# Performance work log

Hardware: AMD Instinct MI355X
Metric: run time of the kernel (lower is better)

## Reference

```python
import jax, jax.numpy as jnp
import numpy as np

IN_DIM = 128; OUT_DIM = 128; H = 8; DK = OUT_DIM // H
N_A = 100000; N_B = 100000; E0 = 400000; E1 = 400000
NUM_TYPES = 2; NUM_REL = 2
EPS = 1e-9; LN_EPS = 1e-5


def setup_inputs() -> dict:
    key = jax.random.key(0)
    ks = jax.random.split(key, 16)
    s = 0.02
    xav = float(np.sqrt(6.0 / (DK + DK)))  # xavier_uniform bound for (dk, dk)
    inp = {}
    inp['x_a'] = jax.random.normal(ks[0], (N_A, IN_DIM), jnp.float32)
    inp['x_b'] = jax.random.normal(ks[1], (N_B, IN_DIM), jnp.float32)
    inp['ew0'] = jax.random.uniform(ks[2], (E0,), jnp.float32)
    inp['ew1'] = jax.random.uniform(ks[3], (E1,), jnp.float32)
    inp['src0'] = jax.random.randint(ks[4], (E0,), 0, N_A)
    inp['dst0'] = jax.random.randint(ks[5], (E0,), 0, N_B)
    inp['src1'] = jax.random.randint(ks[6], (E1,), 0, N_B)
    inp['dst1'] = jax.random.randint(ks[7], (E1,), 0, N_A)
    # per-node-type stacked linear params: [type, in, out]
    inp['Wk'] = jax.random.normal(ks[8], (NUM_TYPES, IN_DIM, OUT_DIM), jnp.float32) * s
    inp['bk'] = jnp.zeros((NUM_TYPES, OUT_DIM), jnp.float32)
    inp['Wq'] = jax.random.normal(ks[9], (NUM_TYPES, IN_DIM, OUT_DIM), jnp.float32) * s
    inp['bq'] = jnp.zeros((NUM_TYPES, OUT_DIM), jnp.float32)
    inp['Wv'] = jax.random.normal(ks[10], (NUM_TYPES, IN_DIM, OUT_DIM), jnp.float32) * s
    inp['bv'] = jnp.zeros((NUM_TYPES, OUT_DIM), jnp.float32)
    inp['Wa'] = jax.random.normal(ks[11], (NUM_TYPES, OUT_DIM, OUT_DIM), jnp.float32) * s
    inp['ba'] = jnp.zeros((NUM_TYPES, OUT_DIM), jnp.float32)
    inp['ln_g'] = jnp.ones((NUM_TYPES, OUT_DIM), jnp.float32)
    inp['ln_b'] = jnp.zeros((NUM_TYPES, OUT_DIM), jnp.float32)
    inp['rel_pri'] = jnp.ones((NUM_REL, H), jnp.float32)
    inp['rel_att'] = jax.random.uniform(ks[12], (NUM_REL, H, DK, DK), jnp.float32, -xav, xav)
    inp['rel_msg'] = jax.random.uniform(ks[13], (NUM_REL, H, DK, DK), jnp.float32, -xav, xav)
    inp['skip'] = jnp.ones((NUM_TYPES,), jnp.float32)
    return inp


def _edge_softmax(logits, dst, n_dst):
    # segment softmax over incoming edges of each dst node; logits: (E, H)
    m = jax.ops.segment_max(logits, dst, num_segments=n_dst)
    e = jnp.exp(logits - m[dst])
    s = jax.ops.segment_sum(e, dst, num_segments=n_dst)
    return e / s[dst]


def _relation(x_s, x_d, src, dst, ew, Wk_s, bk_s, Wq_d, bq_d, Wv_s, bv_s,
              ratt, rmsg, rpri, n_dst):
    # per-relation HGT attention -> aggregated dst messages (n_dst, H, DK)
    k = (x_s @ Wk_s + bk_s).reshape(-1, H, DK)
    k = jnp.einsum('nhd,hde->nhe', k, ratt)
    v = (x_s @ Wv_s + bv_s).reshape(-1, H, DK)
    v = jnp.einsum('nhd,hde->nhe', v, rmsg)
    q = (x_d @ Wq_d + bq_d).reshape(-1, H, DK)
    t = jnp.einsum('ehd,ehd->eh', q[dst], k[src])  # edge dot score (E, H)
    # dst-normalized edge weight -> additive log bias
    ew = jnp.clip(ew, 0.0)
    den = jax.ops.segment_sum(ew, dst, num_segments=n_dst)
    ewn = ew / jnp.maximum(den[dst], EPS)
    t = t + jnp.log(ewn + EPS)[:, None]
    t = t * rpri / jnp.sqrt(jnp.float32(DK))
    a = _edge_softmax(t, dst, n_dst)  # (E, H)
    msg = v[src] * a[:, :, None]      # (E, H, DK)
    return jax.ops.segment_sum(msg, dst, num_segments=n_dst)


def _forward(x_a, x_b, ew0, ew1, Wk, bk, Wq, bq, Wv, bv, Wa, ba, ln_g, ln_b,
             rel_pri, rel_att, rel_msg, skip, src0, dst0, src1, dst1):
    # relation 0: a -> b (src type 0, dst type 1); relation 1: b -> a
    t_b = _relation(x_a, x_b, src0, dst0, ew0, Wk[0], bk[0], Wq[1], bq[1],
                    Wv[0], bv[0], rel_att[0], rel_msg[0], rel_pri[0], x_b.shape[0])
    t_a = _relation(x_b, x_a, src1, dst1, ew1, Wk[1], bk[1], Wq[0], bq[0],
                    Wv[1], bv[1], rel_att[1], rel_msg[1], rel_pri[1], x_a.shape[0])
    def combine(t, base, nid):
        alpha = jax.nn.sigmoid(skip[nid])
        trans = t.reshape(-1, OUT_DIM) @ Wa[nid] + ba[nid]  # dropout: eval mode
        out = trans * alpha + base * (1.0 - alpha)
        mu = jnp.mean(out, axis=-1, keepdims=True)
        var = jnp.var(out, axis=-1, keepdims=True)
        return (out - mu) / jnp.sqrt(var + LN_EPS) * ln_g[nid] + ln_b[nid]
    return combine(t_a, x_a, 0), combine(t_b, x_b, 1)


def reference(x_a, x_b, ew0, ew1, src0, dst0, src1, dst1, Wk, bk, Wq, bq, Wv, bv,
              Wa, ba, ln_g, ln_b, rel_pri, rel_att, rel_msg, skip):
    return _forward(x_a, x_b, ew0, ew1, Wk, bk, Wq, bq, Wv, bv, Wa, ba, ln_g, ln_b,
                    rel_pri, rel_att, rel_msg, skip, src0, dst0, src1, dst1)
```

## Files before the change

kernel.cpp:

```cpp
#include <hip/hip_runtime.h>
#include <cstdint>
#include <cstddef>

#define EPSF 1e-9f

typedef __bf16 bf16x8 __attribute__((ext_vector_type(8)));
typedef float fvec4 __attribute__((ext_vector_type(4)));

__device__ __forceinline__ float blo(unsigned int u) { return __uint_as_float(u << 16); }
__device__ __forceinline__ float bhi(unsigned int u) { return __uint_as_float(u & 0xffff0000u); }
__device__ __forceinline__ unsigned short f2bf(float f) {
  unsigned int u = __float_as_uint(f);
  u += 0x7fffu + ((u >> 16) & 1u);
  return (unsigned short)(u >> 16);
}
__device__ __forceinline__ unsigned int pack2bf(float a, float b) {
  return (unsigned int)f2bf(a) | ((unsigned int)f2bf(b) << 16);
}

__global__ __launch_bounds__(256) void fzero(float* __restrict__ p, long n) {
  long i = (long)blockIdx.x * blockDim.x + threadIdx.x;
  long stride = (long)gridDim.x * blockDim.x;
  long n4 = n >> 2;
  float4* p4 = (float4*)p;
  for (long j = i; j < n4; j += stride) p4[j] = make_float4(0.f, 0.f, 0.f, 0.f);
  for (long j = (n4 << 2) + i; j < n; j += stride) p[j] = 0.f;
}

__global__ __launch_bounds__(256) void fuse_w(
    const float* __restrict__ Wk, const float* __restrict__ bk,
    const float* __restrict__ Wv, const float* __restrict__ bv,
    const float* __restrict__ rel_att, const float* __restrict__ rel_msg,
    __bf16* __restrict__ WkvT, float* __restrict__ bkvf)
{
  int i = blockIdx.x;
  int t = blockIdx.y;
  int c = threadIdx.x;
  int m = c >> 7, cc = c & 127;
  int h = cc >> 4, e = cc & 15;
  const float* R = (m ? rel_msg : rel_att) + t * 2048 + h * 256;
  const float* srcW = (m ? Wv : Wk) + t * 16384;
  const float* srcB = (m ? bv : bk) + t * 128;
  const float* row = (i < 128) ? (srcW + i * 128) : srcB;
  float acc = 0.f;
#pragma unroll
  for (int d = 0; d < 16; ++d) acc = fmaf(row[h * 16 + d], R[d * 16 + e], acc);
  if (i < 128) WkvT[(size_t)t * 32768 + (size_t)c * 128 + i] = (__bf16)acc;
  else         bkvf[t * 256 + c] = acc;
}

__global__ __launch_bounds__(128) void cvt_wT(
    const float* __restrict__ Wq, const float* __restrict__ Wa,
    __bf16* __restrict__ WqT, __bf16* __restrict__ WaT)
{
  int k = blockIdx.x, t = blockIdx.y, c = threadIdx.x;
  const float* src = (blockIdx.z ? Wa : Wq) + t * 16384 + k * 128 + c;
  __bf16* dst = (blockIdx.z ? WaT : WqT) + t * 16384 + c * 128 + k;
  dst[0] = (__bf16)src[0];
}

__global__ __launch_bounds__(256) void gemm_mfma(
    const float* __restrict__ A, int M,
    const __bf16* __restrict__ WT, const float* __restrict__ bias,
    __bf16* __restrict__ C, int ldc)
{
  int tid = threadIdx.x, l = tid & 63, wid = tid >> 6;
  int l15 = l & 15, l4 = l >> 4;
  int rowb = blockIdx.x * 64 + (wid & 1) * 32;
  int colb = blockIdx.y * 128 + (wid >> 1) * 64;

  fvec4 z = {0.f, 0.f, 0.f, 0.f};
  fvec4 acc[2][4];
#pragma unroll
  for (int m = 0; m < 2; ++m)
#pragma unroll
    for (int n = 0; n < 4; ++n) acc[m][n] = z;

#pragma unroll
  for (int ks = 0; ks < 4; ++ks) {
    int kb = ks * 32 + l4 * 8;
    bf16x8 af[2], bfr[4];
#pragma unroll
    for (int m = 0; m < 2; ++m) {
      int r = rowb + m * 16 + l15;
      r = r < M ? r : M - 1;
      const float4* ap = (const float4*)(A + (size_t)r * 128 + kb);
      float4 a0 = ap[0], a1 = ap[1];
      bf16x8 v;
      v[0] = (__bf16)a0.x; v[1] = (__bf16)a0.y; v[2] = (__bf16)a0.z; v[3] = (__bf16)a0.w;
      v[4] = (__bf16)a1.x; v[5] = (__bf16)a1.y; v[6] = (__bf16)a1.z; v[7] = (__bf16)a1.w;
      af[m] = v;
    }
#pragma unroll
    for (int n = 0; n < 4; ++n)
      bfr[n] = *(const bf16x8*)(WT + (size_t)(colb + n * 16 + l15) * 128 + kb);
#pragma unroll
    for (int m = 0; m < 2; ++m)
#pragma unroll
      for (int n = 0; n < 4; ++n)
        acc[m][n] = __builtin_amdgcn_mfma_f32_16x16x32_bf16(af[m], bfr[n], acc[m][n], 0, 0, 0);
  }

#pragma unroll
  for (int m = 0; m < 2; ++m)
#pragma unroll
    for (int n = 0; n < 4; ++n) {
      int col = colb + n * 16 + l15;
      float bcol = bias[col];
#pragma unroll
      for (int reg = 0; reg < 4; ++reg) {
        int r = rowb + m * 16 + l4 * 4 + reg;
        if (r < M) C[(size_t)r * ldc + col] = (__bf16)(acc[m][n][reg] + bcol);
      }
    }
}

__global__ __launch_bounds__(256) void csr_count2(
    const int* __restrict__ dst0, int E0, const int* __restrict__ dst1, int E1,
    int* __restrict__ deg, int NB)
{
  int e = blockIdx.x * 256 + threadIdx.x;
  if (e < E0) atomicAdd(&deg[dst0[e]], 1);
  else if (e < E0 + E1) atomicAdd(&deg[NB + dst1[e - E0]], 1);
}

__global__ __launch_bounds__(256) void csr_partial(
    const int* __restrict__ deg, int N, int* __restrict__ partial)
{
  int base = blockIdx.x * 1024 + threadIdx.x * 4;
  int s = 0;
#pragma unroll
  for (int i = 0; i < 4; ++i) if (base + i < N) s += deg[base + i];
#pragma unroll
  for (int m = 1; m < 64; m <<= 1) s += __shfl_xor(s, m, 64);
  __shared__ int wsum[4];
  if ((threadIdx.x & 63) == 0) wsum[threadIdx.x >> 6] = s;
  __syncthreads();
  if (threadIdx.x == 0) partial[blockIdx.x] = wsum[0] + wsum[1] + wsum[2] + wsum[3];
}

__global__ void csr_scan_partials(const int* __restrict__ partial,
                                  int* __restrict__ pscan, int NP)
{
  if (blockIdx.x == 0 && threadIdx.x == 0) {
    int s = 0;
    for (int i = 0; i < NP; ++i) { pscan[i] = s; s += partial[i]; }
  }
}

__global__ __launch_bounds__(256) void csr_scan_chunk(
    const int* __restrict__ deg, const int* __restrict__ pscan,
    int* __restrict__ row_start, int* __restrict__ cursor, int N)
{
  __shared__ int ls[256];
  int base = blockIdx.x * 1024 + threadIdx.x * 4;
  int v0 = 0, v1 = 0, v2 = 0, v3 = 0;
  if (base + 0 < N) v0 = deg[base + 0];
  if (base + 1 < N) v1 = deg[base + 1];
  if (base + 2 < N) v2 = deg[base + 2];
  if (base + 3 < N) v3 = deg[base + 3];
  int s = v0 + v1 + v2 + v3;
  ls[threadIdx.x] = s;
  __syncthreads();
  for (int off = 1; off < 256; off <<= 1) {
    int t = (threadIdx.x >= off) ? ls[threadIdx.x - off] : 0;
    __syncthreads();
    ls[threadIdx.x] += t;
    __syncthreads();
  }
  int excl = pscan[blockIdx.x] + ls[threadIdx.x] - s;
  int p0 = excl, p1 = excl + v0, p2 = excl + v0 + v1, p3 = excl + v0 + v1 + v2;
  if (base + 0 < N) { row_start[base + 0] = p0; cursor[base + 0] = p0; }
  if (base + 1 < N) { row_start[base + 1] = p1; cursor[base + 1] = p1; }
  if (base + 2 < N) { row_start[base + 2] = p2; cursor[base + 2] = p2; }
  if (base + 3 < N) { row_start[base + 3] = p3; cursor[base + 3] = p3; }
}

__global__ __launch_bounds__(256) void csr_scatter2(
    const int* __restrict__ dst0, const int* __restrict__ src0, const float* __restrict__ ew0, int E0,
    const int* __restrict__ dst1, const int* __restrict__ src1, const float* __restrict__ ew1, int E1,
    int* __restrict__ cursor, int* __restrict__ sidx, float* __restrict__ ewc, int NB)
{
  int e = blockIdx.x * 256 + threadIdx.x;
  if (e < E0) {
    int p = atomicAdd(&cursor[dst0[e]], 1);
    sidx[p] = src0[e];
    ewc[p] = fmaxf(ew0[e], 0.f);
  } else if (e < E0 + E1) {
    int e1 = e - E0;
    int p = atomicAdd(&cursor[NB + dst1[e1]], 1);
    sidx[p] = src1[e1];
    ewc[p] = fmaxf(ew1[e1], 0.f);
  }
}

__device__ __forceinline__ void proc_edge(
    float qlo, float qhi, unsigned int ku, unsigned int vu, float w,
    float inv_den, float pr, float& s, float2& acc)
{
  float t = qlo * blo(ku) + qhi * bhi(ku);
  t += __shfl_xor(t, 1, 64);
  t += __shfl_xor(t, 2, 64);
  t += __shfl_xor(t, 4, 64);
  float x = __expf((t + __logf(w * inv_den + EPSF)) * pr);
  s += x;
  acc.x = fmaf(x, blo(vu), acc.x);
  acc.y = fmaf(x, bhi(vu), acc.y);
}

__global__ __launch_bounds__(256) void hgt_dst(
    const __bf16* __restrict__ kvsb, const __bf16* __restrict__ qb,
    const int* __restrict__ row_start, const int* __restrict__ deg,
    const int* __restrict__ sidx, const float* __restrict__ ewc,
    const float* __restrict__ pri8,
    __bf16* __restrict__ agg, int N)
{
  const unsigned short* kvs = (const unsigned short*)kvsb;
  int n = (blockIdx.x * 256 + threadIdx.x) >> 6;
  int lane = threadIdx.x & 63;
  if (n >= N) return;
  int c0 = lane * 2;
  unsigned int* out = (unsigned int*)(agg + (size_t)n * 128 + c0);
  int d = deg[n];
  if (d == 0) { out[0] = 0u; return; }
  int base = row_start[n];

  float ds = 0.f;
  for (int j = lane; j < d; j += 64) ds += ewc[base + j];
#pragma unroll
  for (int m = 1; m < 64; m <<= 1) ds += __shfl_xor(ds, m, 64);
  float inv_den = 1.f / fmaxf(ds, EPSF);

  int h = lane >> 3;
  float pr = pri8[h] * 0.25f;
  unsigned int qu = *(const unsigned int*)((const unsigned short*)qb + (size_t)n * 128 + c0);
  float qlo = blo(qu), qhi = bhi(qu);

  float s = 0.f;
  float2 acc = make_float2(0.f, 0.f);
  int j = 0;
  for (; j + 4 <= d; j += 4) {
    int b = base + j;
    int si0 = sidx[b], si1 = sidx[b + 1], si2 = sidx[b + 2], si3 = sidx[b + 3];
    float w0 = ewc[b], w1 = ewc[b + 1], w2 = ewc[b + 2], w3 = ewc[b + 3];
    const unsigned short* p0 = kvs + (size_t)si0 * 256 + c0;
    const unsigned short* p1 = kvs + (size_t)si1 * 256 + c0;
    const unsigned short* p2 = kvs + (size_t)si2 * 256 + c0;
    const unsigned short* p3 = kvs + (size_t)si3 * 256 + c0;
    unsigned int k0 = *(const unsigned int*)p0, v0 = *(const unsigned int*)(p0 + 128);
    unsigned int k1 = *(const unsigned int*)p1, v1 = *(const unsigned int*)(p1 + 128);
    unsigned int k2 = *(const unsigned int*)p2, v2 = *(const unsigned int*)(p2 + 128);
    unsigned int k3 = *(const unsigned int*)p3, v3 = *(const unsigned int*)(p3 + 128);
    proc_edge(qlo, qhi, k0, v0, w0, inv_den, pr, s, acc);
    proc_edge(qlo, qhi, k1, v1, w1, inv_den, pr, s, acc);
    proc_edge(qlo, qhi, k2, v2, w2, inv_den, pr, s, acc);
    proc_edge(qlo, qhi, k3, v3, w3, inv_den, pr, s, acc);
  }
  for (; j < d; ++j) {
    int b = base + j;
    const unsigned short* p = kvs + (size_t)sidx[b] * 256 + c0;
    proc_edge(qlo, qhi, *(const unsigned int*)p, *(const unsigned int*)(p + 128),
              ewc[b], inv_den, pr, s, acc);
  }
  float is = 1.f / s;
  out[0] = pack2bf(acc.x * is, acc.y * is);
}

__global__ __launch_bounds__(256) void wa_ln(
    const __bf16* __restrict__ Ag, const __bf16* __restrict__ WT,
    const float* __restrict__ bias, const float* __restrict__ xbase,
    const float* __restrict__ g, const float* __restrict__ bb,
    const float* __restrict__ skip, float* __restrict__ out, int M)
{
  int tid = threadIdx.x, l = tid & 63, wid = tid >> 6;
  int l15 = l & 15, l4 = l >> 4;
  int rowb = blockIdx.x * 64 + wid * 16;

  fvec4 z = {0.f, 0.f, 0.f, 0.f};
  fvec4 acc[8];
#pragma unroll
  for (int n = 0; n < 8; ++n) acc[n] = z;

#pragma unroll
  for (int ks = 0; ks < 4; ++ks) {
    int kb = ks * 32 + l4 * 8;
    int r = rowb + l15;
    r = r < M ? r : M - 1;
    bf16x8 af = *(const bf16x8*)(Ag + (size_t)r * 128 + kb);
#pragma unroll
    for (int n = 0; n < 8; ++n) {
      bf16x8 bfr = *(const bf16x8*)(WT + (size_t)(n * 16 + l15) * 128 + kb);
      acc[n] = __builtin_amdgcn_mfma_f32_16x16x32_bf16(af, bfr, acc[n], 0, 0, 0);
    }
  }

  float alpha = 1.f / (1.f + __expf(-skip[0]));
  float onema = 1.f - alpha;
  float o[8][4];
  float psum[4] = {0.f, 0.f, 0.f, 0.f};
  float psq[4] = {0.f, 0.f, 0.f, 0.f};
#pragma unroll
  for (int n = 0; n < 8; ++n) {
    int col = n * 16 + l15;
    float bcol = bias[col];
#pragma unroll
    for (int reg = 0; reg < 4; ++reg) {
      int r = rowb + l4 * 4 + reg;
      float xv = (r < M) ? xbase[(size_t)r * 128 + col] : 0.f;
      float val = (acc[n][reg] + bcol) * alpha + xv * onema;
      o[n][reg] = val;
      psum[reg] += val;
      psq[reg] = fmaf(val, val, psq[reg]);
    }
  }
#pragma unroll
  for (int reg = 0; reg < 4; ++reg) {
#pragma unroll
    for (int m = 1; m < 16; m <<= 1) {
      psum[reg] += __shfl_xor(psum[reg], m, 64);
      psq[reg] += __shfl_xor(psq[reg], m, 64);
    }
  }
  float mu[4], is[4];
#pragma unroll
  for (int reg = 0; reg < 4; ++reg) {
    mu[reg] = psum[reg] * (1.f / 128.f);
    float var = psq[reg] * (1.f / 128.f) - mu[reg] * mu[reg];
    is[reg] = 1.f / sqrtf(var + 1e-5f);
  }
#pragma unroll
  for (int n = 0; n < 8; ++n) {
    int col = n * 16 + l15;
    float gc = g[col], bc = bb[col];
#pragma unroll
    for (int reg = 0; reg < 4; ++reg) {
      int r = rowb + l4 * 4 + reg;
      if (r < M) out[(size_t)r * 128 + col] = (o[n][reg] - mu[reg]) * is[reg] * gc + bc;
    }
  }
}

extern "C" void kernel_launch(void* const* d_in, const int* in_sizes, int n_in,
                              void* d_out, int out_size, void* d_ws, size_t ws_size,
                              hipStream_t stream)
{
  const float* x_a = (const float*)d_in[0];
  const float* x_b = (const float*)d_in[1];
  const float* ew0 = (const float*)d_in[2];
  const float* ew1 = (const float*)d_in[3];
  const int* src0 = (const int*)d_in[4];
  const int* dst0 = (const int*)d_in[5];
  const int* src1 = (const int*)d_in[6];
  const int* dst1 = (const int*)d_in[7];
  const float* Wk = (const float*)d_in[8];
  const float* bk = (const float*)d_in[9];
  const float* Wq = (const float*)d_in[10];
  const float* bq = (const float*)d_in[11];
  const float* Wv = (const float*)d_in[12];
  const float* bv = (const float*)d_in[13];
  const float* Wa = (const float*)d_in[14];
  const float* ba = (const float*)d_in[15];
  const float* ln_g = (const float*)d_in[16];
  const float* ln_b = (const float*)d_in[17];
  const float* rel_pri = (const float*)d_in[18];
  const float* rel_att = (const float*)d_in[19];
  const float* rel_msg = (const float*)d_in[20];
  const float* skip = (const float*)d_in[21];

  int NA = in_sizes[0] / 128, NB = in_sizes[1] / 128;
  int E0 = in_sizes[2], E1 = in_sizes[3];
  int NMAX = NA > NB ? NA : NB;
  int NM = (NMAX + 255) & ~255;
  int N2 = NA + NB;
  int N2M = (N2 + 255) & ~255;
  int E2 = E0 + E1;
  int E2M = (E2 + 255) & ~255;

  char* wsbase = (char*)d_ws;
  size_t off = 0;
  auto alloc = [&](size_t bytes) { char* p = wsbase + off; off += (bytes + 255) & ~(size_t)255; return p; };
  __bf16* kvb   = (__bf16*)alloc((size_t)NM * 256 * 2);
  __bf16* qd    = (__bf16*)alloc((size_t)NM * 128 * 2);
  __bf16* agg_a = (__bf16*)alloc((size_t)NM * 128 * 2);
  __bf16* agg_b = (__bf16*)alloc((size_t)NM * 128 * 2);
  __bf16* WkvT  = (__bf16*)alloc(2 * 256 * 128 * 2);
  __bf16* WqT   = (__bf16*)alloc(2 * 128 * 128 * 2);
  __bf16* WaT   = (__bf16*)alloc(2 * 128 * 128 * 2);
  float* bkvf   = (float*)alloc(2 * 256 * 4);
  int* deg      = (int*)alloc((size_t)N2M * 4);
  int* row_st   = (int*)alloc((size_t)N2M * 4);
  int* cur      = (int*)alloc((size_t)N2M * 4);
  int* partial  = (int*)alloc(1024 * 4);
  int* pscan    = (int*)alloc(1024 * 4);
  int* sidx     = (int*)alloc((size_t)E2M * 4);
  float* ewc    = (float*)alloc((size_t)E2M * 4);

  float* outf = (float*)d_out;
  dim3 b256(256);
  auto cdiv = [](int a, int b) { return (unsigned)((a + b - 1) / b); };

  fuse_w<<<dim3(129, 2), b256, 0, stream>>>(Wk, bk, Wv, bv, rel_att, rel_msg, WkvT, bkvf);
  cvt_wT<<<dim3(128, 2, 2), 128, 0, stream>>>(Wq, Wa, WqT, WaT);

  int NP = (N2 + 1023) / 1024;
  fzero<<<64, b256, 0, stream>>>((float*)deg, N2);
  csr_count2<<<cdiv(E2, 256), b256, 0, stream>>>(dst0, E0, dst1, E1, deg, NB);
  csr_partial<<<NP, b256, 0, stream>>>(deg, N2, partial);
  csr_scan_partials<<<1, 64, 0, stream>>>(partial, pscan, NP);
  csr_scan_chunk<<<NP, b256, 0, stream>>>(deg, pscan, row_st, cur, N2);
  csr_scatter2<<<cdiv(E2, 256), b256, 0, stream>>>(dst0, src0, ew0, E0,
                                                   dst1, src1, ew1, E1,
                                                   cur, sidx, ewc, NB);

  gemm_mfma<<<dim3(cdiv(NA, 64), 2), b256, 0, stream>>>(x_a, NA, WkvT, bkvf, kvb, 256);
  gemm_mfma<<<dim3(cdiv(NB, 64), 1), b256, 0, stream>>>(x_b, NB, WqT + 16384, bq + 128, qd, 128);
  hgt_dst<<<cdiv(NB, 4), b256, 0, stream>>>(kvb, qd, row_st, deg, sidx, ewc,
                                            rel_pri, agg_b, NB);

  gemm_mfma<<<dim3(cdiv(NB, 64), 2), b256, 0, stream>>>(x_b, NB, WkvT + 32768, bkvf + 256, kvb, 256);
  gemm_mfma<<<dim3(cdiv(NA, 64), 1), b256, 0, stream>>>(x_a, NA, WqT, bq, qd, 128);
  hgt_dst<<<cdiv(NA, 4), b256, 0, stream>>>(kvb, qd, row_st + NB, deg + NB, sidx, ewc,
                                            rel_pri + 8, agg_a, NA);

  wa_ln<<<cdiv(NA, 64), b256, 0, stream>>>(agg_a, WaT, ba, x_a, ln_g, ln_b, skip, outf, NA);
  wa_ln<<<cdiv(NB, 64), b256, 0, stream>>>(agg_b, WaT + 16384, ba + 128, x_b,
                                           ln_g + 128, ln_b + 128, skip + 1,
                                           outf + (size_t)NA * 128, NB);
}
```

Before: 693.2 us.

## Fuse K/V/Q projections per node type into one LDS-staged MFMA GEMM

Concatenates the fused K/V weights and the Q weights for each node type into one 384-column transposed matrix. Each 64-row input tile is loaded from fp32 once, converted to bf16 and staged in swizzled shared memory, then reused across all three 128-column output groups. Previously each node feature matrix was read and converted twice (once for KV, once for Q) across four GEMM launches. The trade-off is separate KV/Q buffers per type (more workspace) and larger per-thread register fragments.

```diff
diff --git a/kernel.cpp b/kernel.cpp
--- a/kernel.cpp
+++ b/kernel.cpp
@@ -31,7 +31,7 @@
     const float* __restrict__ Wk, const float* __restrict__ bk,
     const float* __restrict__ Wv, const float* __restrict__ bv,
     const float* __restrict__ rel_att, const float* __restrict__ rel_msg,
-    __bf16* __restrict__ WkvT, float* __restrict__ bkvf)
+    __bf16* __restrict__ WkvqT, float* __restrict__ bkvq)
 {
   int i = blockIdx.x;
   int t = blockIdx.y;
@@ -45,74 +45,105 @@
   float acc = 0.f;
 #pragma unroll
   for (int d = 0; d < 16; ++d) acc = fmaf(row[h * 16 + d], R[d * 16 + e], acc);
-  if (i < 128) WkvT[(size_t)t * 32768 + (size_t)c * 128 + i] = (__bf16)acc;
-  else         bkvf[t * 256 + c] = acc;
+  if (i < 128) WkvqT[(size_t)t * 49152 + (size_t)c * 128 + i] = (__bf16)acc;
+  else         bkvq[t * 384 + c] = acc;
 }
 
 __global__ __launch_bounds__(128) void cvt_wT(
-    const float* __restrict__ Wq, const float* __restrict__ Wa,
-    __bf16* __restrict__ WqT, __bf16* __restrict__ WaT)
+    const float* __restrict__ Wq, const float* __restrict__ bq,
+    const float* __restrict__ Wa,
+    __bf16* __restrict__ WkvqT, __bf16* __restrict__ WaT,
+    float* __restrict__ bkvq)
 {
   int k = blockIdx.x, t = blockIdx.y, c = threadIdx.x;
-  const float* src = (blockIdx.z ? Wa : Wq) + t * 16384 + k * 128 + c;
-  __bf16* dst = (blockIdx.z ? WaT : WqT) + t * 16384 + c * 128 + k;
-  dst[0] = (__bf16)src[0];
-}
-
-__global__ __launch_bounds__(256) void gemm_mfma(
+  if (blockIdx.z == 0) {
+    WkvqT[(size_t)t * 49152 + (size_t)(256 + c) * 128 + k] = (__bf16)Wq[t * 16384 + k * 128 + c];
+    if (k == 0) bkvq[t * 384 + 256 + c] = bq[t * 128 + c];
+  } else {
+    WaT[(size_t)t * 16384 + (size_t)c * 128 + k] = (__bf16)Wa[t * 16384 + k * 128 + c];
+  }
+}
+
+__global__ __launch_bounds__(256) void gemm_kvq(
     const float* __restrict__ A, int M,
     const __bf16* __restrict__ WT, const float* __restrict__ bias,
-    __bf16* __restrict__ C, int ldc)
-{
-  int tid = threadIdx.x, l = tid & 63, wid = tid >> 6;
-  int l15 = l & 15, l4 = l >> 4;
-  int rowb = blockIdx.x * 64 + (wid & 1) * 32;
-  int colb = blockIdx.y * 128 + (wid >> 1) * 64;
-
-  fvec4 z = {0.f, 0.f, 0.f, 0.f};
-  fvec4 acc[2][4];
+    __bf16* __restrict__ KV, __bf16* __restrict__ Q)
+{
+  __shared__ __bf16 As[64 * 128];
+  const int tid = threadIdx.x;
+  const int rowb = blockIdx.x * 64;
+
+#pragma unroll
+  for (int i = 0; i < 4; ++i) {
+    int f = tid + i * 256;
+    int r = f >> 4;
+    int ch = f & 15;
+    int gr = rowb + r; gr = gr < M ? gr : M - 1;
+    const float4* ap = (const float4*)(A + (size_t)gr * 128 + ch * 8);
+    float4 a0 = ap[0], a1 = ap[1];
+    bf16x8 v;
+    v[0] = (__bf16)a0.x; v[1] = (__bf16)a0.y; v[2] = (__bf16)a0.z; v[3] = (__bf16)a0.w;
+    v[4] = (__bf16)a1.x; v[5] = (__bf16)a1.y; v[6] = (__bf16)a1.z; v[7] = (__bf16)a1.w;
+    int sw = (ch * 16) ^ ((r & 7) << 4);
+    *(bf16x8*)((char*)As + r * 256 + sw) = v;
+  }
+  __syncthreads();
+
+  const int l = tid & 63, wid = tid >> 6;
+  const int l15 = l & 15, l4 = l >> 4;
+  const int wm = wid & 1, wn = wid >> 1;
+
+  bf16x8 af[2][4];
 #pragma unroll
   for (int m = 0; m < 2; ++m)
 #pragma unroll
-    for (int n = 0; n < 4; ++n) acc[m][n] = z;
-
-#pragma unroll
-  for (int ks = 0; ks < 4; ++ks) {
-    int kb = ks * 32 + l4 * 8;
-    bf16x8 af[2], bfr[4];
-#pragma unroll
-    for (int m = 0; m < 2; ++m) {
-      int r = rowb + m * 16 + l15;
-      r = r < M ? r : M - 1;
-      const float4* ap = (const float4*)(A + (size_t)r * 128 + kb);
-      float4 a0 = ap[0], a1 = ap[1];
-      bf16x8 v;
-      v[0] = (__bf16)a0.x; v[1] = (__bf16)a0.y; v[2] = (__bf16)a0.z; v[3] = (__bf16)a0.w;
-      v[4] = (__bf16)a1.x; v[5] = (__bf16)a1.y; v[6] = (__bf16)a1.z; v[7] = (__bf16)a1.w;
-      af[m] = v;
+    for (int ks = 0; ks < 4; ++ks) {
+      int r = wm * 32 + m * 16 + l15;
+      int off = (ks * 64 + l4 * 16) ^ ((r & 7) << 4);
+      af[m][ks] = *(const bf16x8*)((const char*)As + r * 256 + off);
     }
+
+#pragma unroll
+  for (int t = 0; t < 3; ++t) {
+    const int colb = t * 128 + wn * 64;
+    fvec4 z = {0.f, 0.f, 0.f, 0.f};
+    fvec4 acc[2][4];
+#pragma unroll
+    for (int m = 0; m < 2; ++m)
+#pragma unroll
+      for (int n = 0; n < 4; ++n) acc[m][n] = z;
+
+    bf16x8 bfr[4][4];
 #pragma unroll
     for (int n = 0; n < 4; ++n)
-      bfr[n] = *(const bf16x8*)(WT + (size_t)(colb + n * 16 + l15) * 128 + kb);
+#pragma unroll
+      for (int ks = 0; ks < 4; ++ks)
+        bfr[n][ks] = *(const bf16x8*)(WT + (size_t)(colb + n * 16 + l15) * 128 + ks * 32 + l4 * 8);
+
+#pragma unroll
+    for (int ks = 0; ks < 4; ++ks)
+#pragma unroll
+      for (int m = 0; m < 2; ++m)
+#pragma unroll
+        for (int n = 0; n < 4; ++n)
+          acc[m][n] = __builtin_amdgcn_mfma_f32_16x16x32_bf16(af[m][ks], bfr[n][ks], acc[m][n], 0, 0, 0);
+
+    __bf16* Cp = (t < 2) ? KV : Q;
+    const int ldc = (t < 2) ? 256 : 128;
+    const int cbase = (t < 2) ? colb : wn * 64;
 #pragma unroll
     for (int m = 0; m < 2; ++m)
 #pragma unroll
-      for (int n = 0; n < 4; ++n)
-        acc[m][n] = __builtin_amdgcn_mfma_f32_16x16x32_bf16(af[m], bfr[n], acc[m][n], 0, 0, 0);
-  }
-
-#pragma unroll
-  for (int m = 0; m < 2; ++m)
-#pragma unroll
-    for (int n = 0; n < 4; ++n) {
-      int col = colb + n * 16 + l15;
-      float bcol = bias[col];
-#pragma unroll
-      for (int reg = 0; reg < 4; ++reg) {
-        int r = rowb + m * 16 + l4 * 4 + reg;
-        if (r < M) C[(size_t)r * ldc + col] = (__bf16)(acc[m][n][reg] + bcol);
+      for (int n = 0; n < 4; ++n) {
+        int col = cbase + n * 16 + l15;
+        float bcol = bias[colb + n * 16 + l15];
+#pragma unroll
+        for (int reg = 0; reg < 4; ++reg) {
+          int r = rowb + wm * 32 + m * 16 + l4 * 4 + reg;
+          if (r < M) Cp[(size_t)r * ldc + col] = (__bf16)(acc[m][n][reg] + bcol);
+        }
       }
-    }
+  }
 }
 
 __global__ __launch_bounds__(256) void csr_count2(
@@ -379,14 +410,15 @@
   char* wsbase = (char*)d_ws;
   size_t off = 0;
   auto alloc = [&](size_t bytes) { char* p = wsbase + off; off += (bytes + 255) & ~(size_t)255; return p; };
-  __bf16* kvb   = (__bf16*)alloc((size_t)NM * 256 * 2);
-  __bf16* qd    = (__bf16*)alloc((size_t)NM * 128 * 2);
+  __bf16* kvb_a = (__bf16*)alloc((size_t)NM * 256 * 2);
+  __bf16* kvb_b = (__bf16*)alloc((size_t)NM * 256 * 2);
+  __bf16* qd_a  = (__bf16*)alloc((size_t)NM * 128 * 2);
+  __bf16* qd_b  = (__bf16*)alloc((size_t)NM * 128 * 2);
   __bf16* agg_a = (__bf16*)alloc((size_t)NM * 128 * 2);
   __bf16* agg_b = (__bf16*)alloc((size_t)NM * 128 * 2);
-  __bf16* WkvT  = (__bf16*)alloc(2 * 256 * 128 * 2);
-  __bf16* WqT   = (__bf16*)alloc(2 * 128 * 128 * 2);
+  __bf16* WkvqT = (__bf16*)alloc(2 * 384 * 128 * 2);
   __bf16* WaT   = (__bf16*)alloc(2 * 128 * 128 * 2);
-  float* bkvf   = (float*)alloc(2 * 256 * 4);
+  float* bkvq   = (float*)alloc(2 * 384 * 4);
   int* deg      = (int*)alloc((size_t)N2M * 4);
   int* row_st   = (int*)alloc((size_t)N2M * 4);
   int* cur      = (int*)alloc((size_t)N2M * 4);
@@ -399,8 +431,8 @@
   dim3 b256(256);
   auto cdiv = [](int a, int b) { return (unsigned)((a + b - 1) / b); };
 
-  fuse_w<<<dim3(129, 2), b256, 0, stream>>>(Wk, bk, Wv, bv, rel_att, rel_msg, WkvT, bkvf);
-  cvt_wT<<<dim3(128, 2, 2), 128, 0, stream>>>(Wq, Wa, WqT, WaT);
+  fuse_w<<<dim3(129, 2), b256, 0, stream>>>(Wk, bk, Wv, bv, rel_att, rel_msg, WkvqT, bkvq);
+  cvt_wT<<<dim3(128, 2, 2), 128, 0, stream>>>(Wq, bq, Wa, WkvqT, WaT, bkvq);
 
   int NP = (N2 + 1023) / 1024;
   fzero<<<64, b256, 0, stream>>>((float*)deg, N2);
@@ -412,14 +444,12 @@
                                                    dst1, src1, ew1, E1,
                                                    cur, sidx, ewc, NB);
 
-  gemm_mfma<<<dim3(cdiv(NA, 64), 2), b256, 0, stream>>>(x_a, NA, WkvT, bkvf, kvb, 256);
-  gemm_mfma<<<dim3(cdiv(NB, 64), 1), b256, 0, stream>>>(x_b, NB, WqT + 16384, bq + 128, qd, 128);
-  hgt_dst<<<cdiv(NB, 4), b256, 0, stream>>>(kvb, qd, row_st, deg, sidx, ewc,
+  gemm_kvq<<<cdiv(NA, 64), b256, 0, stream>>>(x_a, NA, WkvqT, bkvq, kvb_a, qd_a);
+  gemm_kvq<<<cdiv(NB, 64), b256, 0, stream>>>(x_b, NB, WkvqT + 49152, bkvq + 384, kvb_b, qd_b);
+
+  hgt_dst<<<cdiv(NB, 4), b256, 0, stream>>>(kvb_a, qd_b, row_st, deg, sidx, ewc,
                                             rel_pri, agg_b, NB);
-
-  gemm_mfma<<<dim3(cdiv(NB, 64), 2), b256, 0, stream>>>(x_b, NB, WkvT + 32768, bkvf + 256, kvb, 256);
-  gemm_mfma<<<dim3(cdiv(NA, 64), 1), b256, 0, stream>>>(x_a, NA, WqT, bq, qd, 128);
-  hgt_dst<<<cdiv(NA, 4), b256, 0, stream>>>(kvb, qd, row_st + NB, deg + NB, sidx, ewc,
+  hgt_dst<<<cdiv(NA, 4), b256, 0, stream>>>(kvb_b, qd_a, row_st + NB, deg + NB, sidx, ewc,
                                             rel_pri + 8, agg_a, NA);
 
   wa_ln<<<cdiv(NA, 64), b256, 0, stream>>>(agg_a, WaT, ba, x_a, ln_g, ln_b, skip, outf, NA);
```

New measurement: 627.3 us. 9.5% less time.
